# Optimization experiments

Hardware: AMD Instinct MI355X
Metric: run time of the kernel (lower is better)

Reference implementation:

```python
import jax, jax.numpy as jnp
import numpy as np

B, I, H = 8192, 1024, 1024

def _xavier(key, out_f, in_f):
    limit = (6.0 / (in_f + out_f)) ** 0.5
    return jax.random.uniform(key, (out_f, in_f), jnp.float32, -limit, limit)

def setup_inputs() -> dict:
    key = jax.random.key(0)
    ks = jax.random.split(key, 11)
    inp = {
        'x': jax.random.normal(ks[0], (B, I), jnp.float32),
        'h': jax.random.normal(ks[1], (B, H), jnp.float32),
        'c': jax.random.normal(ks[2], (B, H), jnp.float32),
    }
    names = ['Wxi', 'Whi', 'Wxf', 'Whf', 'Wxo', 'Who', 'Wxg', 'Whg']
    for n, k in zip(names, ks[3:]):
        in_f = I if n[1] == 'x' else H
        inp[n + '_w'] = _xavier(k, H, in_f)
        inp[n + '_b'] = jnp.zeros((H,), jnp.float32)
    return inp

def reference(x, h, c,
              Wxi_w, Wxi_b, Whi_w, Whi_b,
              Wxf_w, Wxf_b, Whf_w, Whf_b,
              Wxo_w, Wxo_b, Who_w, Who_b,
              Wxg_w, Wxg_b, Whg_w, Whg_b):
    Wx = jnp.concatenate([Wxi_w, Wxf_w, Wxo_w, Wxg_w], axis=0)  # [4H, I]
    Wh = jnp.concatenate([Whi_w, Whf_w, Who_w, Whg_w], axis=0)  # [4H, H]
    bx = jnp.concatenate([Wxi_b, Wxf_b, Wxo_b, Wxg_b], axis=0)  # [4H]
    bh = jnp.concatenate([Whi_b, Whf_b, Who_b, Whg_b], axis=0)  # [4H]
    z = x @ Wx.T + bx + h @ Wh.T + bh  # [B, 4H]
    zi, zf, zo, zg = jnp.split(z, 4, axis=-1)
    it = jax.nn.sigmoid(zi)
    ft = jax.nn.sigmoid(zf)
    ot = jax.nn.sigmoid(zo)
    gt = jnp.tanh(zg)
    c_next = ft * c + it * gt
    h_next = ot * jnp.tanh(c_next)
    return (h_next, c_next)
```

## Files before the change

### kernel.cpp

```cpp
#include <hip/hip_runtime.h>
#include <hip/hip_bf16.h>
#include <cstdint>


typedef __bf16 bf16;
typedef __attribute__((ext_vector_type(8))) bf16 bf16x8;
typedef __attribute__((ext_vector_type(4))) bf16 bf16x4;
typedef __attribute__((ext_vector_type(4))) float f32x4;

#define BM 128
#define BN 128
#define BK 32
#define CN_OFF 8388608

__device__ __forceinline__ void gload_lds16(const void* g, void* l) {
  __builtin_amdgcn_global_load_lds(
      (__attribute__((address_space(1))) void*)(void*)(g),
      (__attribute__((address_space(3))) void*)(void*)(l),
      16, 0, 0);
}

__global__ __launch_bounds__(256) void pack_all(
    const float* __restrict__ x, const float* __restrict__ h,
    const float* __restrict__ wxi, const float* __restrict__ whi,
    const float* __restrict__ wxf, const float* __restrict__ whf,
    const float* __restrict__ wxo, const float* __restrict__ who,
    const float* __restrict__ wxg, const float* __restrict__ whg,
    const float* __restrict__ bxi, const float* __restrict__ bhi,
    const float* __restrict__ bxf, const float* __restrict__ bhf,
    const float* __restrict__ bxo, const float* __restrict__ bho,
    const float* __restrict__ bxg, const float* __restrict__ bhg,
    bf16* __restrict__ A, bf16* __restrict__ W, float* __restrict__ Bcomb) {
  int b = blockIdx.x;
  if (b < 16384) {
    int idx = b * 256 + threadIdx.x;
    int m = idx >> 9;
    int k = (idx & 511) * 4;
    const float* src = (k < 1024) ? (x + (size_t)m * 1024 + k)
                                  : (h + (size_t)m * 1024 + (k - 1024));
    f32x4 v = *(const f32x4*)src;
    bf16x4 o;
    o[0] = (bf16)v[0]; o[1] = (bf16)v[1]; o[2] = (bf16)v[2]; o[3] = (bf16)v[3];
    *(bf16x4*)(A + (size_t)idx * 4) = o;
  } else {
    int idx = (b - 16384) * 256 + threadIdx.x;
    int n = idx >> 9;
    int k = (idx & 511) * 4;
    int gate = (n >> 4) & 3;
    int j    = (n >> 6) * 16 + (n & 15);
    const float* wx = (gate == 0) ? wxi : (gate == 1) ? wxf : (gate == 2) ? wxo : wxg;
    const float* wh = (gate == 0) ? whi : (gate == 1) ? whf : (gate == 2) ? who : whg;
    const float* src = (k < 1024) ? (wx + (size_t)j * 1024 + k)
                                  : (wh + (size_t)j * 1024 + (k - 1024));
    f32x4 v = *(const f32x4*)src;
    bf16x4 o;
    o[0] = (bf16)v[0]; o[1] = (bf16)v[1]; o[2] = (bf16)v[2]; o[3] = (bf16)v[3];
    *(bf16x4*)(W + (size_t)idx * 4) = o;
    if ((idx & 511) == 0) {
      const float* bx = (gate == 0) ? bxi : (gate == 1) ? bxf : (gate == 2) ? bxo : bxg;
      const float* bh = (gate == 0) ? bhi : (gate == 1) ? bhf : (gate == 2) ? bho : bhg;
      Bcomb[n] = bx[j] + bh[j];
    }
  }
}

__device__ __forceinline__ float sigf(float v) { return 1.f / (1.f + __expf(-v)); }
__device__ __forceinline__ float tanhfast(float v) {
  v = fminf(15.f, fmaxf(-15.f, v));
  float e = __expf(2.f * v);
  return (e - 1.f) / (e + 1.f);
}

__global__ __launch_bounds__(256) void gemm_lstm(const bf16* __restrict__ A,
                                                 const bf16* __restrict__ W,
                                                 const float* __restrict__ Bcomb,
                                                 const float* __restrict__ c,
                                                 float* __restrict__ out) {
  constexpr int K = 2048;
  __shared__ __align__(16) bf16 As[BM * BK];
  __shared__ __align__(16) bf16 Bs[BN * BK];

  const int t    = threadIdx.x;
  const int wave = t >> 6;
  const int lane = t & 63;
  const int m0 = blockIdx.y * BM;
  const int n0 = blockIdx.x * BN;
  const int wm = (wave >> 1) * 64;
  const int wn = (wave & 1) * 64;
  const int lrow = lane & 15;
  const int lkg  = lane >> 4;

  f32x4 acc[4][4] = {};

  const int arow = t >> 2;
  const int acol = (t & 3) * 8;
  const bf16* gA0 = A + (size_t)(m0 + arow) * K + acol;
  const bf16* gA1 = A + (size_t)(m0 + 64 + arow) * K + acol;
  const bf16* gB0 = W + (size_t)(n0 + arow) * K + acol;
  const bf16* gB1 = W + (size_t)(n0 + 64 + arow) * K + acol;
  bf16* lA0 = &As[t * 8];
  bf16* lA1 = &As[2048 + t * 8];
  bf16* lB0 = &Bs[t * 8];
  bf16* lB1 = &Bs[2048 + t * 8];

  for (int kt = 0; kt < K; kt += BK) {
    gload_lds16(gA0 + kt, lA0);
    gload_lds16(gA1 + kt, lA1);
    gload_lds16(gB0 + kt, lB0);
    gload_lds16(gB1 + kt, lB1);
    __syncthreads();

    bf16x8 a[4], b[4];
#pragma unroll
    for (int i = 0; i < 4; ++i) {
      a[i] = *(const bf16x8*)&As[(wm + i * 16 + lrow) * BK + lkg * 8];
      b[i] = *(const bf16x8*)&Bs[(wn + i * 16 + lrow) * BK + lkg * 8];
    }
#pragma unroll
    for (int mi = 0; mi < 4; ++mi)
#pragma unroll
      for (int ni = 0; ni < 4; ++ni)
        acc[mi][ni] = __builtin_amdgcn_mfma_f32_16x16x32_bf16(a[mi], b[ni], acc[mi][ni], 0, 0, 0);
    __syncthreads();
  }

  const int jg = (blockIdx.x * 2 + (wn >> 6)) * 16 + lrow;
  const float bi = Bcomb[n0 + wn +  0 + lrow];
  const float bf_ = Bcomb[n0 + wn + 16 + lrow];
  const float bo = Bcomb[n0 + wn + 32 + lrow];
  const float bg = Bcomb[n0 + wn + 48 + lrow];

#pragma unroll
  for (int mi = 0; mi < 4; ++mi) {
    const int row0 = m0 + wm + mi * 16 + lkg * 4;
    float cv[4];
#pragma unroll
    for (int r = 0; r < 4; ++r)
      cv[r] = c[(size_t)(row0 + r) * 1024 + jg];
#pragma unroll
    for (int r = 0; r < 4; ++r) {
      float zi = acc[mi][0][r] + bi;
      float zf = acc[mi][1][r] + bf_;
      float zo = acc[mi][2][r] + bo;
      float zg = acc[mi][3][r] + bg;
      float it = sigf(zi), ft = sigf(zf), ot = sigf(zo), gt = tanhfast(zg);
      float cn = ft * cv[r] + it * gt;
      size_t off = (size_t)(row0 + r) * 1024 + jg;
      out[off] = ot * tanhfast(cn);
      out[CN_OFF + off] = cn;
    }
  }
}

extern "C" void kernel_launch(void* const* d_in, const int* in_sizes, int n_in,
                              void* d_out, int out_size, void* d_ws, size_t ws_size,
                              hipStream_t stream) {
  const float* x   = (const float*)d_in[0];
  const float* h   = (const float*)d_in[1];
  const float* c   = (const float*)d_in[2];
  const float* Wxi = (const float*)d_in[3];  const float* bxi = (const float*)d_in[4];
  const float* Whi = (const float*)d_in[5];  const float* bhi = (const float*)d_in[6];
  const float* Wxf = (const float*)d_in[7];  const float* bxf = (const float*)d_in[8];
  const float* Whf = (const float*)d_in[9];  const float* bhf = (const float*)d_in[10];
  const float* Wxo = (const float*)d_in[11]; const float* bxo = (const float*)d_in[12];
  const float* Who = (const float*)d_in[13]; const float* bho = (const float*)d_in[14];
  const float* Wxg = (const float*)d_in[15]; const float* bxg = (const float*)d_in[16];
  const float* Whg = (const float*)d_in[17]; const float* bhg = (const float*)d_in[18];
  float* out = (float*)d_out;

  bf16*  Abuf  = (bf16*)d_ws;
  bf16*  Wbuf  = Abuf + (size_t)8192 * 2048;
  float* Bcomb = (float*)(Wbuf + (size_t)4096 * 2048);

  pack_all<<<24576, 256, 0, stream>>>(x, h,
                                      Wxi, Whi, Wxf, Whf, Wxo, Who, Wxg, Whg,
                                      bxi, bhi, bxf, bhf, bxo, bho, bxg, bhg,
                                      Abuf, Wbuf, Bcomb);
  gemm_lstm<<<dim3(32, 64), 256, 0, stream>>>(Abuf, Wbuf, Bcomb, c, out);
}
```

Baseline: 378.3 us.

## Pre-swizzle operands into MFMA fragment order and load directly to registers

The pack kernel now writes A and W in a per-wave, per-k-tile fragment layout, so each lane's bf16x8 MFMA operand sits contiguously. The GEMM drops LDS staging and barriers entirely and streams fragments from global memory into registers with a two-stage double buffer. Without LDS sharing, each wave fetches its own operands, so the two waves sharing an M or N slice read the same data from global memory or cache twice. The pack kernel also handles 8 elements per thread, halving its grid.

Result: faster. 355.3 us (-6.1%).

```diff
diff --git a/kernel.cpp b/kernel.cpp
--- a/kernel.cpp
+++ b/kernel.cpp
@@ -5,20 +5,9 @@
 
 typedef __bf16 bf16;
 typedef __attribute__((ext_vector_type(8))) bf16 bf16x8;
-typedef __attribute__((ext_vector_type(4))) bf16 bf16x4;
 typedef __attribute__((ext_vector_type(4))) float f32x4;
 
-#define BM 128
-#define BN 128
-#define BK 32
 #define CN_OFF 8388608
-
-__device__ __forceinline__ void gload_lds16(const void* g, void* l) {
-  __builtin_amdgcn_global_load_lds(
-      (__attribute__((address_space(1))) void*)(void*)(g),
-      (__attribute__((address_space(3))) void*)(void*)(l),
-      16, 0, 0);
-}
 
 __global__ __launch_bounds__(256) void pack_all(
     const float* __restrict__ x, const float* __restrict__ h,
@@ -30,36 +19,49 @@
     const float* __restrict__ bxf, const float* __restrict__ bhf,
     const float* __restrict__ bxo, const float* __restrict__ bho,
     const float* __restrict__ bxg, const float* __restrict__ bhg,
-    bf16* __restrict__ A, bf16* __restrict__ W, float* __restrict__ Bcomb) {
+    bf16* __restrict__ A2, bf16* __restrict__ B2, float* __restrict__ Bcomb) {
   int b = blockIdx.x;
-  if (b < 16384) {
-    int idx = b * 256 + threadIdx.x;
-    int m = idx >> 9;
-    int k = (idx & 511) * 4;
+  if (b < 8192) {
+    int chunk = b * 256 + threadIdx.x;
+    int lane = chunk & 63;
+    int mi   = (chunk >> 6) & 3;
+    int wm   = (chunk >> 8) & 1;
+    int kt   = (chunk >> 9) & 63;
+    int mb   = chunk >> 15;
+    int m = mb * 128 + wm * 64 + mi * 16 + (lane & 15);
+    int k = kt * 32 + (lane >> 4) * 8;
     const float* src = (k < 1024) ? (x + (size_t)m * 1024 + k)
                                   : (h + (size_t)m * 1024 + (k - 1024));
-    f32x4 v = *(const f32x4*)src;
-    bf16x4 o;
-    o[0] = (bf16)v[0]; o[1] = (bf16)v[1]; o[2] = (bf16)v[2]; o[3] = (bf16)v[3];
-    *(bf16x4*)(A + (size_t)idx * 4) = o;
+    f32x4 v0 = *(const f32x4*)src;
+    f32x4 v1 = *(const f32x4*)(src + 4);
+    bf16x8 o;
+    o[0]=(bf16)v0[0]; o[1]=(bf16)v0[1]; o[2]=(bf16)v0[2]; o[3]=(bf16)v0[3];
+    o[4]=(bf16)v1[0]; o[5]=(bf16)v1[1]; o[6]=(bf16)v1[2]; o[7]=(bf16)v1[3];
+    *(bf16x8*)(A2 + (size_t)chunk * 8) = o;
   } else {
-    int idx = (b - 16384) * 256 + threadIdx.x;
-    int n = idx >> 9;
-    int k = (idx & 511) * 4;
-    int gate = (n >> 4) & 3;
-    int j    = (n >> 6) * 16 + (n & 15);
+    int chunk = (b - 8192) * 256 + threadIdx.x;
+    int lane = chunk & 63;
+    int gate = (chunk >> 6) & 3;
+    int wn   = (chunk >> 8) & 1;
+    int kt   = (chunk >> 9) & 63;
+    int nb   = chunk >> 15;
+    int jl = lane & 15;
+    int j  = (nb * 2 + wn) * 16 + jl;
+    int k  = kt * 32 + (lane >> 4) * 8;
     const float* wx = (gate == 0) ? wxi : (gate == 1) ? wxf : (gate == 2) ? wxo : wxg;
     const float* wh = (gate == 0) ? whi : (gate == 1) ? whf : (gate == 2) ? who : whg;
     const float* src = (k < 1024) ? (wx + (size_t)j * 1024 + k)
                                   : (wh + (size_t)j * 1024 + (k - 1024));
-    f32x4 v = *(const f32x4*)src;
-    bf16x4 o;
-    o[0] = (bf16)v[0]; o[1] = (bf16)v[1]; o[2] = (bf16)v[2]; o[3] = (bf16)v[3];
-    *(bf16x4*)(W + (size_t)idx * 4) = o;
-    if ((idx & 511) == 0) {
+    f32x4 v0 = *(const f32x4*)src;
+    f32x4 v1 = *(const f32x4*)(src + 4);
+    bf16x8 o;
+    o[0]=(bf16)v0[0]; o[1]=(bf16)v0[1]; o[2]=(bf16)v0[2]; o[3]=(bf16)v0[3];
+    o[4]=(bf16)v1[0]; o[5]=(bf16)v1[1]; o[6]=(bf16)v1[2]; o[7]=(bf16)v1[3];
+    *(bf16x8*)(B2 + (size_t)chunk * 8) = o;
+    if (kt == 0 && (lane >> 4) == 0) {
       const float* bx = (gate == 0) ? bxi : (gate == 1) ? bxf : (gate == 2) ? bxo : bxg;
       const float* bh = (gate == 0) ? bhi : (gate == 1) ? bhf : (gate == 2) ? bho : bhg;
-      Bcomb[n] = bx[j] + bh[j];
+      Bcomb[(nb * 2 + wn) * 64 + gate * 16 + jl] = bx[j] + bh[j];
     }
   }
 }
@@ -71,68 +73,79 @@
   return (e - 1.f) / (e + 1.f);
 }
 
-__global__ __launch_bounds__(256) void gemm_lstm(const bf16* __restrict__ A,
-                                                 const bf16* __restrict__ W,
+__global__ __launch_bounds__(256) void gemm_lstm(const bf16* __restrict__ A2,
+                                                 const bf16* __restrict__ B2,
                                                  const float* __restrict__ Bcomb,
                                                  const float* __restrict__ c,
                                                  float* __restrict__ out) {
-  constexpr int K = 2048;
-  __shared__ __align__(16) bf16 As[BM * BK];
-  __shared__ __align__(16) bf16 Bs[BN * BK];
-
   const int t    = threadIdx.x;
   const int wave = t >> 6;
   const int lane = t & 63;
-  const int m0 = blockIdx.y * BM;
-  const int n0 = blockIdx.x * BN;
-  const int wm = (wave >> 1) * 64;
-  const int wn = (wave & 1) * 64;
+  const int nb = blockIdx.x;
+  const int mb = blockIdx.y;
+  const int wm = wave >> 1;
+  const int wn = wave & 1;
   const int lrow = lane & 15;
   const int lkg  = lane >> 4;
 
+  const bf16* pa = A2 + (size_t)mb * 262144 + wm * 2048 + lane * 8;
+  const bf16* pb = B2 + (size_t)nb * 262144 + wn * 2048 + lane * 8;
+
   f32x4 acc[4][4] = {};
+  bf16x8 a0[4], b0[4], a1[4], b1[4];
 
-  const int arow = t >> 2;
-  const int acol = (t & 3) * 8;
-  const bf16* gA0 = A + (size_t)(m0 + arow) * K + acol;
-  const bf16* gA1 = A + (size_t)(m0 + 64 + arow) * K + acol;
-  const bf16* gB0 = W + (size_t)(n0 + arow) * K + acol;
-  const bf16* gB1 = W + (size_t)(n0 + 64 + arow) * K + acol;
-  bf16* lA0 = &As[t * 8];
-  bf16* lA1 = &As[2048 + t * 8];
-  bf16* lB0 = &Bs[t * 8];
-  bf16* lB1 = &Bs[2048 + t * 8];
+#pragma unroll
+  for (int i = 0; i < 4; ++i) {
+    a0[i] = *(const bf16x8*)(pa + i * 512);
+    b0[i] = *(const bf16x8*)(pb + i * 512);
+  }
+#pragma unroll
+  for (int i = 0; i < 4; ++i) {
+    a1[i] = *(const bf16x8*)(pa + 4096 + i * 512);
+    b1[i] = *(const bf16x8*)(pb + 4096 + i * 512);
+  }
 
-  for (int kt = 0; kt < K; kt += BK) {
-    gload_lds16(gA0 + kt, lA0);
-    gload_lds16(gA1 + kt, lA1);
-    gload_lds16(gB0 + kt, lB0);
-    gload_lds16(gB1 + kt, lB1);
-    __syncthreads();
-
-    bf16x8 a[4], b[4];
+  for (int kt = 0; kt < 64; kt += 2) {
 #pragma unroll
-    for (int i = 0; i < 4; ++i) {
-      a[i] = *(const bf16x8*)&As[(wm + i * 16 + lrow) * BK + lkg * 8];
-      b[i] = *(const bf16x8*)&Bs[(wn + i * 16 + lrow) * BK + lkg * 8];
+    for (int mi = 0; mi < 4; ++mi)
+#pragma unroll
+      for (int ni = 0; ni < 4; ++ni)
+        acc[mi][ni] = __builtin_amdgcn_mfma_f32_16x16x32_bf16(a0[mi], b0[ni], acc[mi][ni], 0, 0, 0);
+    if (kt + 2 < 64) {
+      const bf16* qa = pa + (size_t)(kt + 2) * 4096;
+      const bf16* qb = pb + (size_t)(kt + 2) * 4096;
+#pragma unroll
+      for (int i = 0; i < 4; ++i) {
+        a0[i] = *(const bf16x8*)(qa + i * 512);
+        b0[i] = *(const bf16x8*)(qb + i * 512);
+      }
     }
 #pragma unroll
     for (int mi = 0; mi < 4; ++mi)
 #pragma unroll
       for (int ni = 0; ni < 4; ++ni)
-        acc[mi][ni] = __builtin_amdgcn_mfma_f32_16x16x32_bf16(a[mi], b[ni], acc[mi][ni], 0, 0, 0);
-    __syncthreads();
+        acc[mi][ni] = __builtin_amdgcn_mfma_f32_16x16x32_bf16(a1[mi], b1[ni], acc[mi][ni], 0, 0, 0);
+    if (kt + 3 < 64) {
+      const bf16* qa = pa + (size_t)(kt + 3) * 4096;
+      const bf16* qb = pb + (size_t)(kt + 3) * 4096;
+#pragma unroll
+      for (int i = 0; i < 4; ++i) {
+        a1[i] = *(const bf16x8*)(qa + i * 512);
+        b1[i] = *(const bf16x8*)(qb + i * 512);
+      }
+    }
   }
 
-  const int jg = (blockIdx.x * 2 + (wn >> 6)) * 16 + lrow;
-  const float bi = Bcomb[n0 + wn +  0 + lrow];
-  const float bf_ = Bcomb[n0 + wn + 16 + lrow];
-  const float bo = Bcomb[n0 + wn + 32 + lrow];
-  const float bg = Bcomb[n0 + wn + 48 + lrow];
+  const int jg = (nb * 2 + wn) * 16 + lrow;
+  const int bbase = (nb * 2 + wn) * 64 + lrow;
+  const float bi  = Bcomb[bbase +  0];
+  const float bf_ = Bcomb[bbase + 16];
+  const float bo  = Bcomb[bbase + 32];
+  const float bg  = Bcomb[bbase + 48];
 
 #pragma unroll
   for (int mi = 0; mi < 4; ++mi) {
-    const int row0 = m0 + wm + mi * 16 + lkg * 4;
+    const int row0 = mb * 128 + wm * 64 + mi * 16 + lkg * 4;
     float cv[4];
 #pragma unroll
     for (int r = 0; r < 4; ++r)
@@ -172,7 +185,7 @@
   bf16*  Wbuf  = Abuf + (size_t)8192 * 2048;
   float* Bcomb = (float*)(Wbuf + (size_t)4096 * 2048);
 
-  pack_all<<<24576, 256, 0, stream>>>(x, h,
+  pack_all<<<12288, 256, 0, stream>>>(x, h,
                                       Wxi, Whi, Wxf, Whf, Wxo, Who, Wxg, Whg,
                                       bxi, bhi, bxf, bhf, bxo, bho, bxg, bhg,
                                       Abuf, Wbuf, Bcomb);
```
